# Performance work log

Hardware: AMD Instinct MI355X
Metric: run time of the kernel (lower is better)

Reference implementation:

```python
import jax, jax.numpy as jnp
import numpy as np

HEADS = 16
HEAD_DIM = 64
DIM = 1024
INNER = HEADS * HEAD_DIM
EPS = 1e-5


def setup_inputs() -> dict:
    key = jax.random.key(0)
    ks = jax.random.split(key, 7)
    s_qkv = (2.0 / (DIM + 3 * INNER)) ** 0.5
    s_out = (2.0 / (INNER + DIM)) ** 0.5
    return {
        "x": jax.random.normal(ks[0], (4, 2048, DIM), dtype=jnp.float32),
        "w_qkv": jax.random.normal(ks[1], (DIM, 3 * INNER), dtype=jnp.float32) * s_qkv,
        "b_qkv": jnp.zeros((3 * INNER,), dtype=jnp.float32),
        "w_out": jax.random.normal(ks[2], (INNER, DIM), dtype=jnp.float32) * s_out,
        "b_out": jnp.zeros((DIM,), dtype=jnp.float32),
        "ln_gamma": jnp.ones((DIM,), dtype=jnp.float32),
        "ln_beta": jnp.zeros((DIM,), dtype=jnp.float32),
    }


def reference(x, w_qkv, b_qkv, w_out, b_out, ln_gamma, ln_beta):
    # Pre-norm LayerNorm
    mu = jnp.mean(x, axis=-1, keepdims=True)
    var = jnp.var(x, axis=-1, keepdims=True)
    xn = (x - mu) * jax.lax.rsqrt(var + EPS) * ln_gamma + ln_beta
    # QKV projection: [b, l, 3*inner]
    qkv = xn @ w_qkv + b_qkv
    q, k, v = jnp.split(qkv, 3, axis=-1)
    b, l, _ = x.shape
    def heads(t):  # [b, l, inner] -> [b, h, l, d]
        return t.reshape(b, l, HEADS, HEAD_DIM).transpose(0, 2, 1, 3)
    q, k, v = heads(q), heads(k), heads(v)
    scale = HEAD_DIM ** -0.5
    scores = jnp.einsum('bhqd,bhkd->bhqk', q, k) * scale
    att = jax.nn.softmax(scores, axis=-1)
    out = jnp.einsum('bhqk,bhkd->bhqd', att, v)
    out = out.transpose(0, 2, 1, 3).reshape(b, l, INNER)
    return out @ w_out + b_out
```

## Files before the change

kernel.cpp:

```cpp
#include <hip/hip_runtime.h>
#include <stdint.h>

typedef __bf16 bf16;
typedef bf16 bf16x4 __attribute__((ext_vector_type(4)));
typedef bf16 bf16x8 __attribute__((ext_vector_type(8)));
typedef float f32x4 __attribute__((ext_vector_type(4)));


__device__ __forceinline__ void gll16(const bf16* g, const bf16* l) {
  __builtin_amdgcn_global_load_lds(
      (__attribute__((address_space(1))) void*)(g),
      (__attribute__((address_space(3))) void*)(l),
      16, 0, 0);
}

__global__ __launch_bounds__(256) void ln_kernel(
    const float* __restrict__ x, const float* __restrict__ gamma,
    const float* __restrict__ beta, bf16* __restrict__ xn)
{
  __shared__ float red[8];
  const long row = blockIdx.x;
  const int t = threadIdx.x;
  f32x4 f = *(const f32x4*)(x + row * 1024 + t * 4);
  float sum = f[0] + f[1] + f[2] + f[3];
  float sq  = f[0]*f[0] + f[1]*f[1] + f[2]*f[2] + f[3]*f[3];
#pragma unroll
  for (int sh = 1; sh < 64; sh <<= 1) {
    sum += __shfl_xor(sum, sh, 64);
    sq  += __shfl_xor(sq,  sh, 64);
  }
  const int wave = t >> 6, lane = t & 63;
  if (lane == 0) { red[wave] = sum; red[wave + 4] = sq; }
  __syncthreads();
  sum = red[0] + red[1] + red[2] + red[3];
  sq  = red[4] + red[5] + red[6] + red[7];
  const float mu  = sum * (1.0f / 1024.0f);
  const float var = sq * (1.0f / 1024.0f) - mu * mu;
  const float rs  = rsqrtf(var + 1e-5f);
  f32x4 g = *(const f32x4*)(gamma + t * 4);
  f32x4 bb = *(const f32x4*)(beta + t * 4);
  bf16x4 ov;
#pragma unroll
  for (int i = 0; i < 4; i++)
    ov[i] = (bf16)((f[i] - mu) * rs * g[i] + bb[i]);
  *(bf16x4*)(xn + row * 1024 + t * 4) = ov;
}

__global__ __launch_bounds__(256) void transpose2_kernel(
    const float* __restrict__ wqkv, bf16* __restrict__ wqkvT,
    const float* __restrict__ wout, bf16* __restrict__ woutT)
{
  __shared__ bf16 tile[32][33];
  const int bx = blockIdx.x;
  const float* in;
  bf16* out;
  int Cc, c0;
  if (bx < 96) { in = wqkv; out = wqkvT; Cc = 3072; c0 = bx * 32; }
  else         { in = wout; out = woutT; Cc = 1024; c0 = (bx - 96) * 32; }
  const int r0 = blockIdx.y * 32;
  const int tx = threadIdx.x & 31, ty = threadIdx.x >> 5;
#pragma unroll
  for (int i = 0; i < 32; i += 8)
    tile[ty + i][tx] = (bf16)in[(long)(r0 + ty + i) * Cc + c0 + tx];
  __syncthreads();
#pragma unroll
  for (int i = 0; i < 32; i += 8)
    out[(long)(c0 + ty + i) * 1024 + r0 + tx] = tile[tx][ty + i];
}

__global__ __launch_bounds__(256, 4) void gemm_bt(
    const bf16* __restrict__ A, const bf16* __restrict__ BT,
    const float* __restrict__ bias, float* __restrict__ C,
    bf16* __restrict__ qb, bf16* __restrict__ kb, bf16* __restrict__ vtb,
    int K, int N, int mode)
{
  __shared__ bf16 sA[2][128 * 32];
  __shared__ bf16 sB[2][128 * 32];
  const int t = threadIdx.x;
  const int lane = t & 63;
  const int wave = t >> 6;
  const int wave_u = __builtin_amdgcn_readfirstlane(wave);
  const int quad = lane >> 4;
  const int c16 = lane & 15;
  const int wm = (wave >> 1) * 64;
  const int wn = (wave & 1) * 64;
  const int m0 = blockIdx.x * 128;
  const int n0 = blockIdx.y * 128;

  f32x4 acc[4][4] = {};

  const int srow = t >> 2;
  const int scol = (((t & 3) ^ ((t >> 3) & 3)) * 8);
  const bf16* gA = A + (long)(m0 + srow) * K + scol;
  const bf16* gB = BT + (long)(n0 + srow) * K + scol;
  const long rowskip = (long)64 * K;
  const int ksw = (quad ^ ((c16 >> 1) & 3)) * 8;

  const int S = K >> 5;

  auto stage = [&](int b, int kk) {
    const bf16* lA = sA[0] + b * 4096 + wave_u * 512;
    const bf16* lB = sB[0] + b * 4096 + wave_u * 512;
    const int k0 = kk * 32;
    gll16(gA + k0, lA);
    gll16(gA + k0 + rowskip, lA + 2048);
    gll16(gB + k0, lB);
    gll16(gB + k0 + rowskip, lB + 2048);
  };

  stage(0, 0);

  int cur = 0;
  for (int s = 0; s < S; s++) {
    __syncthreads();
    if (s + 1 < S)
      stage(cur ^ 1, s + 1);
    const bf16* cA = sA[0] + cur * 4096;
    const bf16* cB = sB[0] + cur * 4096;
    bf16x8 af[4], bfr[4];
#pragma unroll
    for (int i = 0; i < 4; i++)
      af[i] = *(const bf16x8*)(cA + (wm + i * 16 + c16) * 32 + ksw);
#pragma unroll
    for (int j = 0; j < 4; j++)
      bfr[j] = *(const bf16x8*)(cB + (wn + j * 16 + c16) * 32 + ksw);
#pragma unroll
    for (int i = 0; i < 4; i++)
#pragma unroll
      for (int j = 0; j < 4; j++)
        acc[i][j] = __builtin_amdgcn_mfma_f32_16x16x32_bf16(af[i], bfr[j], acc[i][j], 0, 0, 0);
    cur ^= 1;
  }

#pragma unroll
  for (int i = 0; i < 4; i++) {
    const int mbase = m0 + wm + i * 16 + quad * 4;
#pragma unroll
    for (int j = 0; j < 4; j++) {
      const int n = n0 + wn + j * 16 + c16;
      const float bv = bias[n];
      if (mode == 0) {
#pragma unroll
        for (int r = 0; r < 4; r++)
          C[(long)(mbase + r) * N + n] = acc[i][j][r] + bv;
      } else {
        const int part = n >> 10;
        const int inner = n & 1023;
        const int h = inner >> 6, d = inner & 63;
#pragma unroll
        for (int r = 0; r < 4; r++) {
          const int m = mbase + r;
          const int b = m >> 11, l = m & 2047;
          const long bh = (long)((b << 4) | h);
          const float v = acc[i][j][r] + bv;
          if (part == 0)      qb [(bh * 2048 + l) * 64 + d] = (bf16)(v * 0.18033688f);
          else if (part == 1) kb [(bh * 2048 + l) * 64 + d] = (bf16)v;
          else                vtb[(bh * 64 + d) * 2048 + l] = (bf16)v;
        }
      }
    }
  }
}

__global__ __launch_bounds__(256, 2) void attn_kernel(
    const bf16* __restrict__ q, const bf16* __restrict__ k,
    const bf16* __restrict__ vt, bf16* __restrict__ att)
{
  __shared__ bf16 sK[128 * 68];
  __shared__ bf16 sVt[64 * 132];

  const int i = blockIdx.x;
  const int xcd = i & 7;
  const int wi = i >> 3;
  const int qt = wi & 7;
  const int bh = xcd * 8 + (wi >> 3);
  const int b = bh >> 4, h = bh & 15;
  const int q0 = qt * 256;
  const int t = threadIdx.x;
  const int wave = t >> 6, lane = t & 63;
  const int quad = lane >> 4, c16 = lane & 15;

  const bf16* qp = q + (long)bh * (2048 * 64);
  const bf16* kp = k + (long)bh * (2048 * 64);
  const bf16* vp = vt + (long)bh * (64 * 2048);

  bf16x8 aq[4][2];
#pragma unroll
  for (int m = 0; m < 4; m++) {
    const bf16* qrow = qp + (long)(q0 + wave * 64 + m * 16 + c16) * 64 + quad * 8;
    aq[m][0] = *(const bf16x8*)(qrow);
    aq[m][1] = *(const bf16x8*)(qrow + 32);
  }

  f32x4 o_acc[4][4] = {};
  f32x4 o_sum[4] = {};
  bf16x8 vones;
#pragma unroll
  for (int z = 0; z < 8; z++) vones[z] = (bf16)1.0f;

  const int kr = t >> 3;
  const int kd = (t & 7) * 8;
  const int vr = t >> 4;
  const int vc = t & 15;
  const int vl = vc * 8;
  const int vD0 = (vc >> 2) * 32 + (vc & 1) * 16 + ((vc >> 1) & 1) * 4;

  bf16x8 kreg[4], vreg[4];
#pragma unroll
  for (int it = 0; it < 4; it++) {
    kreg[it] = *(const bf16x8*)(kp + (long)(it * 32 + kr) * 64 + kd);
    vreg[it] = *(const bf16x8*)(vp + (long)(it * 16 + vr) * 2048 + vl);
  }

  for (int kt = 0; kt < 16; kt++) {
    __syncthreads();
#pragma unroll
    for (int it = 0; it < 4; it++)
      *(bf16x8*)&sK[(it * 32 + kr) * 68 + kd] = kreg[it];
#pragma unroll
    for (int it = 0; it < 4; it++) {
      const bf16x8 v = vreg[it];
      const bf16x4 lo = __builtin_shufflevector(v, v, 0, 1, 2, 3);
      const bf16x4 hi = __builtin_shufflevector(v, v, 4, 5, 6, 7);
      bf16* d = &sVt[(it * 16 + vr) * 132 + vD0];
      *(bf16x4*)(d)     = lo;
      *(bf16x4*)(d + 8) = hi;
    }
    __syncthreads();

    const int kvn = ((kt + 1) & 15) * 128;

#pragma unroll
    for (int ks = 0; ks < 4; ks++) {
      bf16x8 ap[4];
#pragma unroll
      for (int e = 0; e < 2; e++) {
        const int jb = ks * 2 + e;
        const bf16x8 bk0 = *(const bf16x8*)&sK[(jb * 16 + c16) * 68 + quad * 8];
        const bf16x8 bk1 = *(const bf16x8*)&sK[(jb * 16 + c16) * 68 + 32 + quad * 8];
#pragma unroll
        for (int m = 0; m < 4; m++) {
          f32x4 z = {};
          z = __builtin_amdgcn_mfma_f32_16x16x32_bf16(bk0, aq[m][0], z, 0, 0, 0);
          z = __builtin_amdgcn_mfma_f32_16x16x32_bf16(bk1, aq[m][1], z, 0, 0, 0);
#pragma unroll
          for (int r = 0; r < 4; r++)
            ap[m][e * 4 + r] = (bf16)__builtin_amdgcn_exp2f(z[r]);
        }
      }
      if (ks == 1) {
#pragma unroll
        for (int it = 0; it < 4; it++)
          kreg[it] = *(const bf16x8*)(kp + (long)(kvn + it * 32 + kr) * 64 + kd);
      }
      if (ks == 2) {
#pragma unroll
        for (int it = 0; it < 4; it++)
          vreg[it] = *(const bf16x8*)(vp + (long)(it * 16 + vr) * 2048 + kvn + vl);
      }
#pragma unroll
      for (int m = 0; m < 4; m++)
        o_sum[m] = __builtin_amdgcn_mfma_f32_16x16x32_bf16(ap[m], vones, o_sum[m], 0, 0, 0);
#pragma unroll
      for (int jd = 0; jd < 4; jd++) {
        const bf16x8 bv = *(const bf16x8*)&sVt[(jd * 16 + c16) * 132 + ks * 32 + quad * 8];
#pragma unroll
        for (int m = 0; m < 4; m++)
          o_acc[m][jd] = __builtin_amdgcn_mfma_f32_16x16x32_bf16(ap[m], bv, o_acc[m][jd], 0, 0, 0);
      }
    }
  }

#pragma unroll
  for (int m = 0; m < 4; m++) {
#pragma unroll
    for (int r = 0; r < 4; r++) {
      const float inv = 1.0f / o_sum[m][r];
      const long rowbase = ((long)b * 2048 + q0 + wave * 64 + m * 16 + quad * 4 + r) * 1024 + h * 64;
#pragma unroll
      for (int jd = 0; jd < 4; jd++)
        att[rowbase + jd * 16 + c16] = (bf16)(o_acc[m][jd][r] * inv);
    }
  }
}

extern "C" void kernel_launch(void* const* d_in, const int* in_sizes, int n_in,
                              void* d_out, int out_size, void* d_ws, size_t ws_size,
                              hipStream_t stream) {
  (void)in_sizes; (void)n_in; (void)out_size; (void)ws_size;
  const float* x     = (const float*)d_in[0];
  const float* w_qkv = (const float*)d_in[1];
  const float* b_qkv = (const float*)d_in[2];
  const float* w_out = (const float*)d_in[3];
  const float* b_out = (const float*)d_in[4];
  const float* gamma = (const float*)d_in[5];
  const float* beta  = (const float*)d_in[6];
  float* out = (float*)d_out;
  bf16* ws  = (bf16*)d_ws;

  bf16* xn    = ws;
  bf16* wqkvT = ws + 8388608;
  bf16* woutT = wqkvT + 3145728;
  bf16* qbuf  = woutT + 1048576;
  bf16* kbuf  = qbuf + 8388608;
  bf16* vtbuf = kbuf + 8388608;
  bf16* att   = xn;

  transpose2_kernel<<<dim3(128, 32), 256, 0, stream>>>(w_qkv, wqkvT, w_out, woutT);
  ln_kernel<<<dim3(8192), 256, 0, stream>>>(x, gamma, beta, xn);
  gemm_bt<<<dim3(8192 / 128, 3072 / 128), 256, 0, stream>>>(
      xn, wqkvT, b_qkv, (float*)nullptr, qbuf, kbuf, vtbuf, 1024, 3072, 1);
  attn_kernel<<<dim3(512), 256, 0, stream>>>(qbuf, kbuf, vtbuf, att);
  gemm_bt<<<dim3(8192 / 128, 1024 / 128), 256, 0, stream>>>(
      att, woutT, b_out, out, (bf16*)nullptr, (bf16*)nullptr, (bf16*)nullptr, 1024, 1024, 0);
}
```

Before: 269.0 us.

## Store V row-major, transpose in attention LDS, merge prep kernels, add setprio

Result: faster. 256.3 us (median of 2 runs) (-4.7%).

```diff
diff --git a/kernel.cpp b/kernel.cpp
--- a/kernel.cpp
+++ b/kernel.cpp
@@ -14,64 +14,64 @@
       16, 0, 0);
 }
 
-__global__ __launch_bounds__(256) void ln_kernel(
+__global__ __launch_bounds__(256) void prep_kernel(
+    const float* __restrict__ wqkv, bf16* __restrict__ wqkvT,
+    const float* __restrict__ wout, bf16* __restrict__ woutT,
     const float* __restrict__ x, const float* __restrict__ gamma,
     const float* __restrict__ beta, bf16* __restrict__ xn)
 {
+  __shared__ bf16 tile[32][33];
   __shared__ float red[8];
-  const long row = blockIdx.x;
+  const int bid = blockIdx.x;
   const int t = threadIdx.x;
-  f32x4 f = *(const f32x4*)(x + row * 1024 + t * 4);
-  float sum = f[0] + f[1] + f[2] + f[3];
-  float sq  = f[0]*f[0] + f[1]*f[1] + f[2]*f[2] + f[3]*f[3];
-#pragma unroll
-  for (int sh = 1; sh < 64; sh <<= 1) {
-    sum += __shfl_xor(sum, sh, 64);
-    sq  += __shfl_xor(sq,  sh, 64);
-  }
-  const int wave = t >> 6, lane = t & 63;
-  if (lane == 0) { red[wave] = sum; red[wave + 4] = sq; }
-  __syncthreads();
-  sum = red[0] + red[1] + red[2] + red[3];
-  sq  = red[4] + red[5] + red[6] + red[7];
-  const float mu  = sum * (1.0f / 1024.0f);
-  const float var = sq * (1.0f / 1024.0f) - mu * mu;
-  const float rs  = rsqrtf(var + 1e-5f);
-  f32x4 g = *(const f32x4*)(gamma + t * 4);
-  f32x4 bb = *(const f32x4*)(beta + t * 4);
-  bf16x4 ov;
-#pragma unroll
-  for (int i = 0; i < 4; i++)
-    ov[i] = (bf16)((f[i] - mu) * rs * g[i] + bb[i]);
-  *(bf16x4*)(xn + row * 1024 + t * 4) = ov;
-}
-
-__global__ __launch_bounds__(256) void transpose2_kernel(
-    const float* __restrict__ wqkv, bf16* __restrict__ wqkvT,
-    const float* __restrict__ wout, bf16* __restrict__ woutT)
-{
-  __shared__ bf16 tile[32][33];
-  const int bx = blockIdx.x;
-  const float* in;
-  bf16* out;
-  int Cc, c0;
-  if (bx < 96) { in = wqkv; out = wqkvT; Cc = 3072; c0 = bx * 32; }
-  else         { in = wout; out = woutT; Cc = 1024; c0 = (bx - 96) * 32; }
-  const int r0 = blockIdx.y * 32;
-  const int tx = threadIdx.x & 31, ty = threadIdx.x >> 5;
-#pragma unroll
-  for (int i = 0; i < 32; i += 8)
-    tile[ty + i][tx] = (bf16)in[(long)(r0 + ty + i) * Cc + c0 + tx];
-  __syncthreads();
-#pragma unroll
-  for (int i = 0; i < 32; i += 8)
-    out[(long)(c0 + ty + i) * 1024 + r0 + tx] = tile[tx][ty + i];
+  if (bid < 4096) {
+    const int bx = bid & 127, by = bid >> 7;
+    const float* in;
+    bf16* out;
+    int Cc, c0;
+    if (bx < 96) { in = wqkv; out = wqkvT; Cc = 3072; c0 = bx * 32; }
+    else         { in = wout; out = woutT; Cc = 1024; c0 = (bx - 96) * 32; }
+    const int r0 = by * 32;
+    const int tx = t & 31, ty = t >> 5;
+#pragma unroll
+    for (int i = 0; i < 32; i += 8)
+      tile[ty + i][tx] = (bf16)in[(long)(r0 + ty + i) * Cc + c0 + tx];
+    __syncthreads();
+#pragma unroll
+    for (int i = 0; i < 32; i += 8)
+      out[(long)(c0 + ty + i) * 1024 + r0 + tx] = tile[tx][ty + i];
+  } else {
+    const long row = bid - 4096;
+    f32x4 f = *(const f32x4*)(x + row * 1024 + t * 4);
+    float sum = f[0] + f[1] + f[2] + f[3];
+    float sq  = f[0]*f[0] + f[1]*f[1] + f[2]*f[2] + f[3]*f[3];
+#pragma unroll
+    for (int sh = 1; sh < 64; sh <<= 1) {
+      sum += __shfl_xor(sum, sh, 64);
+      sq  += __shfl_xor(sq,  sh, 64);
+    }
+    const int wave = t >> 6, lane = t & 63;
+    if (lane == 0) { red[wave] = sum; red[wave + 4] = sq; }
+    __syncthreads();
+    sum = red[0] + red[1] + red[2] + red[3];
+    sq  = red[4] + red[5] + red[6] + red[7];
+    const float mu  = sum * (1.0f / 1024.0f);
+    const float var = sq * (1.0f / 1024.0f) - mu * mu;
+    const float rs  = rsqrtf(var + 1e-5f);
+    f32x4 g = *(const f32x4*)(gamma + t * 4);
+    f32x4 bb = *(const f32x4*)(beta + t * 4);
+    bf16x4 ov;
+#pragma unroll
+    for (int i = 0; i < 4; i++)
+      ov[i] = (bf16)((f[i] - mu) * rs * g[i] + bb[i]);
+    *(bf16x4*)(xn + row * 1024 + t * 4) = ov;
+  }
 }
 
 __global__ __launch_bounds__(256, 4) void gemm_bt(
     const bf16* __restrict__ A, const bf16* __restrict__ BT,
     const float* __restrict__ bias, float* __restrict__ C,
-    bf16* __restrict__ qb, bf16* __restrict__ kb, bf16* __restrict__ vtb,
+    bf16* __restrict__ qb, bf16* __restrict__ kb, bf16* __restrict__ vb,
     int K, int N, int mode)
 {
   __shared__ bf16 sA[2][128 * 32];
@@ -147,15 +147,14 @@
         const int part = n >> 10;
         const int inner = n & 1023;
         const int h = inner >> 6, d = inner & 63;
+        bf16* dst = (part == 0) ? qb : (part == 1) ? kb : vb;
+        const float scl = (part == 0) ? 0.18033688f : 1.0f;
 #pragma unroll
         for (int r = 0; r < 4; r++) {
           const int m = mbase + r;
           const int b = m >> 11, l = m & 2047;
           const long bh = (long)((b << 4) | h);
-          const float v = acc[i][j][r] + bv;
-          if (part == 0)      qb [(bh * 2048 + l) * 64 + d] = (bf16)(v * 0.18033688f);
-          else if (part == 1) kb [(bh * 2048 + l) * 64 + d] = (bf16)v;
-          else                vtb[(bh * 64 + d) * 2048 + l] = (bf16)v;
+          dst[(bh * 2048 + l) * 64 + d] = (bf16)((acc[i][j][r] + bv) * scl);
         }
       }
     }
@@ -164,7 +163,7 @@
 
 __global__ __launch_bounds__(256, 2) void attn_kernel(
     const bf16* __restrict__ q, const bf16* __restrict__ k,
-    const bf16* __restrict__ vt, bf16* __restrict__ att)
+    const bf16* __restrict__ vb, bf16* __restrict__ att)
 {
   __shared__ bf16 sK[128 * 68];
   __shared__ bf16 sVt[64 * 132];
@@ -182,7 +181,7 @@
 
   const bf16* qp = q + (long)bh * (2048 * 64);
   const bf16* kp = k + (long)bh * (2048 * 64);
-  const bf16* vp = vt + (long)bh * (64 * 2048);
+  const bf16* vp = vb + (long)bh * (2048 * 64);
 
   bf16x8 aq[4][2];
 #pragma unroll
@@ -200,17 +199,18 @@
 
   const int kr = t >> 3;
   const int kd = (t & 7) * 8;
-  const int vr = t >> 4;
-  const int vc = t & 15;
-  const int vl = vc * 8;
-  const int vD0 = (vc >> 2) * 32 + (vc & 1) * 16 + ((vc >> 1) & 1) * 4;
+  const int lr = t >> 1;
+  const int dh = (t & 1) * 32;
+  const int l32 = lr & 31;
+  const int pcol = (lr >> 5) * 32 + ((l32 >> 2) & 3) * 8 + (l32 >> 4) * 4 + (l32 & 3);
 
   bf16x8 kreg[4], vreg[4];
 #pragma unroll
-  for (int it = 0; it < 4; it++) {
+  for (int it = 0; it < 4; it++)
     kreg[it] = *(const bf16x8*)(kp + (long)(it * 32 + kr) * 64 + kd);
-    vreg[it] = *(const bf16x8*)(vp + (long)(it * 16 + vr) * 2048 + vl);
-  }
+#pragma unroll
+  for (int c = 0; c < 4; c++)
+    vreg[c] = *(const bf16x8*)(vp + (long)lr * 64 + dh + c * 8);
 
   for (int kt = 0; kt < 16; kt++) {
     __syncthreads();
@@ -218,14 +218,10 @@
     for (int it = 0; it < 4; it++)
       *(bf16x8*)&sK[(it * 32 + kr) * 68 + kd] = kreg[it];
 #pragma unroll
-    for (int it = 0; it < 4; it++) {
-      const bf16x8 v = vreg[it];
-      const bf16x4 lo = __builtin_shufflevector(v, v, 0, 1, 2, 3);
-      const bf16x4 hi = __builtin_shufflevector(v, v, 4, 5, 6, 7);
-      bf16* d = &sVt[(it * 16 + vr) * 132 + vD0];
-      *(bf16x4*)(d)     = lo;
-      *(bf16x4*)(d + 8) = hi;
-    }
+    for (int c = 0; c < 4; c++)
+#pragma unroll
+      for (int u = 0; u < 8; u++)
+        sVt[(dh + c * 8 + u) * 132 + pcol] = vreg[c][u];
     __syncthreads();
 
     const int kvn = ((kt + 1) & 15) * 128;
@@ -255,9 +251,10 @@
       }
       if (ks == 2) {
 #pragma unroll
-        for (int it = 0; it < 4; it++)
-          vreg[it] = *(const bf16x8*)(vp + (long)(it * 16 + vr) * 2048 + kvn + vl);
-      }
+        for (int c = 0; c < 4; c++)
+          vreg[c] = *(const bf16x8*)(vp + (long)(kvn + lr) * 64 + dh + c * 8);
+      }
+      __builtin_amdgcn_s_setprio(1);
 #pragma unroll
       for (int m = 0; m < 4; m++)
         o_sum[m] = __builtin_amdgcn_mfma_f32_16x16x32_bf16(ap[m], vones, o_sum[m], 0, 0, 0);
@@ -268,6 +265,7 @@
         for (int m = 0; m < 4; m++)
           o_acc[m][jd] = __builtin_amdgcn_mfma_f32_16x16x32_bf16(ap[m], bv, o_acc[m][jd], 0, 0, 0);
       }
+      __builtin_amdgcn_s_setprio(0);
     }
   }
 
@@ -303,14 +301,14 @@
   bf16* woutT = wqkvT + 3145728;
   bf16* qbuf  = woutT + 1048576;
   bf16* kbuf  = qbuf + 8388608;
-  bf16* vtbuf = kbuf + 8388608;
   bf16* att   = xn;
-
-  transpose2_kernel<<<dim3(128, 32), 256, 0, stream>>>(w_qkv, wqkvT, w_out, woutT);
-  ln_kernel<<<dim3(8192), 256, 0, stream>>>(x, gamma, beta, xn);
+  bf16* vb    = (bf16*)d_out;
+
+  prep_kernel<<<dim3(12288), 256, 0, stream>>>(w_qkv, wqkvT, w_out, woutT,
+                                               x, gamma, beta, xn);
   gemm_bt<<<dim3(8192 / 128, 3072 / 128), 256, 0, stream>>>(
-      xn, wqkvT, b_qkv, (float*)nullptr, qbuf, kbuf, vtbuf, 1024, 3072, 1);
-  attn_kernel<<<dim3(512), 256, 0, stream>>>(qbuf, kbuf, vtbuf, att);
+      xn, wqkvT, b_qkv, (float*)nullptr, qbuf, kbuf, vb, 1024, 3072, 1);
+  attn_kernel<<<dim3(512), 256, 0, stream>>>(qbuf, kbuf, vb, att);
   gemm_bt<<<dim3(8192 / 128, 1024 / 128), 256, 0, stream>>>(
       att, woutT, b_out, out, (bf16*)nullptr, (bf16*)nullptr, (bf16*)nullptr, 1024, 1024, 0);
 }
```
